# Kernel tuning notes

Measured on AMD Instinct MI355X. Metric: run time of the kernel, lower is better.

Reference implementation:

```python
import jax, jax.numpy as jnp
import numpy as np

NUM_NODES = 6144
INPUT_DIM = 128
OUTPUT_DIM = 128
NUM_HEADS = 4
HEAD_DIM = OUTPUT_DIM // NUM_HEADS
NEG_INF = -9e15  # mask constant used by the original module


def setup_inputs() -> dict:
    key = jax.random.key(0)
    k_x, k_adj, k_W, k_a = jax.random.split(key, 4)
    x = jax.random.normal(k_x, (NUM_NODES, INPUT_DIM), dtype=jnp.float32)
    adj = jax.random.randint(k_adj, (NUM_NODES, NUM_NODES), 0, 2, dtype=jnp.int32)
    # kaiming-uniform-ish init scale
    W = jax.random.uniform(k_W, (NUM_HEADS, INPUT_DIM, HEAD_DIM), dtype=jnp.float32,
                           minval=-1.0, maxval=1.0) * np.sqrt(6.0 / INPUT_DIM)
    a = jax.random.uniform(k_a, (NUM_HEADS, 2 * HEAD_DIM, 1), dtype=jnp.float32,
                           minval=-1.0, maxval=1.0) * np.sqrt(6.0 / (2 * HEAD_DIM))
    return {"x": x, "adj": adj, "W": W, "a": a}


def reference(x, adj, W, a):
    # x: [N, Din], adj: [N, N] int, W: [H, Din, d], a: [H, 2d, 1]
    H, Din, d = W.shape
    N = x.shape[0]
    h = jnp.einsum('ni,hid->hnd', x, W)               # [H, N, d] per-head projections
    a_dst = a[:, :d, 0]                                # applied to h_j (column / source of message)
    a_src = a[:, d:, 0]                                # applied to h_i (row / destination)
    s_dst = jnp.einsum('hnd,hd->hn', h, a_dst)         # [H, N]
    s_src = jnp.einsum('hnd,hd->hn', h, a_src)         # [H, N]
    # energy[h, i, j] = leaky_relu(a1 . h_j + a2 . h_i), same as concat-attention
    energy = jax.nn.leaky_relu(s_src[:, :, None] + s_dst[:, None, :], negative_slope=0.2)
    energy = jnp.where(adj[None] > 0, energy, NEG_INF)  # [H, N, N]
    attention = jax.nn.softmax(energy, axis=-1)
    h_prime = jnp.einsum('hij,hjd->hid', attention, h)  # [H, N, d]
    # faithful to torch h_prime.view(num_nodes, -1) on a contiguous [H,N,d] tensor
    return jnp.reshape(h_prime, (N, H * d))
```

## Files before the change

kernel.cpp:

```cpp
#include <hip/hip_runtime.h>
#include <stdint.h>

#define N_NODES 6144
#define LOG2E 1.44269504088896f

typedef float f32x4 __attribute__((ext_vector_type(4)));
typedef short short8 __attribute__((ext_vector_type(8)));
typedef unsigned int uint32;

extern "C" __device__ float __ocml_native_exp2_f32(float);

__device__ __forceinline__ unsigned int pack2bf(float a, float b) {
  unsigned int ua = __float_as_uint(a) + 0x8000u;
  unsigned int ub = __float_as_uint(b) + 0x8000u;
  return __builtin_amdgcn_perm(ub, ua, 0x07060302u);
}

__global__ __launch_bounds__(256) void k0_pack(const int* __restrict__ adj,
                                               uint32* __restrict__ maskw) {
  unsigned int id = blockIdx.x * 256 + threadIdx.x;
  const int* src = adj + (size_t)id * 32;
  uint32 bits = 0;
  #pragma unroll
  for (int q = 0; q < 8; ++q) {
    int4 v = *(const int4*)(src + q * 4);
    bits |= (v.x != 0 ? 1u : 0u) << (4 * q);
    bits |= (v.y != 0 ? 1u : 0u) << (4 * q + 1);
    bits |= (v.z != 0 ? 1u : 0u) << (4 * q + 2);
    bits |= (v.w != 0 ? 1u : 0u) << (4 * q + 3);
  }
  maskw[id] = bits;
}

__global__ __launch_bounds__(256) void k1_feat(const float* __restrict__ x,
                                               const float* __restrict__ W,
                                               const float* __restrict__ a,
                                               unsigned short* __restrict__ hfT,
                                               float* __restrict__ s_src2,
                                               float* __restrict__ s_dst2) {
  __shared__ float xl[64][132];
  __shared__ float Wl[64][128];
  int t = threadIdx.x;
  int n0 = blockIdx.x * 64;
  for (int u = t; u < 2048; u += 256) {
    int row = u >> 5, c4 = (u & 31) << 2;
    *(float4*)&xl[row][c4] = *(const float4*)(x + (size_t)(n0 + row) * 128 + c4);
  }
  int cg = t & 31, c0 = cg << 2;
  int ng = t >> 5, nb = ng << 3;
  float acc[8][4] = {};
  for (int ic = 0; ic < 2; ++ic) {
    __syncthreads();
    for (int u = t; u < 2048; u += 256) {
      int ii = u >> 5, c4 = (u & 31) << 2;
      int hh = c4 >> 5, d0 = c4 & 31;
      *(float4*)&Wl[ii][c4] = *(const float4*)(W + hh * 4096 + (ic * 64 + ii) * 32 + d0);
    }
    __syncthreads();
    #pragma unroll 4
    for (int ii = 0; ii < 64; ++ii) {
      float4 wv = *(float4*)&Wl[ii][c0];
      int i = ic * 64 + ii;
      #pragma unroll
      for (int r = 0; r < 8; ++r) {
        float xv = xl[nb + r][i];
        acc[r][0] += xv * wv.x; acc[r][1] += xv * wv.y;
        acc[r][2] += xv * wv.z; acc[r][3] += xv * wv.w;
      }
    }
  }
  __syncthreads();
  unsigned short* tb = (unsigned short*)&xl[0][0];
  float* pb = &Wl[0][0];
  int hh = c0 >> 5, d0 = c0 & 31;
  float4 adv = *(const float4*)(a + hh * 64 + d0);
  float4 asv = *(const float4*)(a + hh * 64 + 32 + d0);
  #pragma unroll
  for (int cc = 0; cc < 4; ++cc) {
    unsigned int* dst = (unsigned int*)(tb + (c0 + cc) * 66 + nb);
    #pragma unroll
    for (int p = 0; p < 4; ++p)
      dst[p] = pack2bf(acc[2 * p][cc], acc[2 * p + 1][cc]);
  }
  #pragma unroll
  for (int r = 0; r < 8; ++r) {
    float pd = acc[r][0] * adv.x + acc[r][1] * adv.y + acc[r][2] * adv.z + acc[r][3] * adv.w;
    float ps = acc[r][0] * asv.x + acc[r][1] * asv.y + acc[r][2] * asv.z + acc[r][3] * asv.w;
    pb[(nb + r) * 33 + cg] = pd;
    pb[2112 + (nb + r) * 33 + cg] = ps;
  }
  __syncthreads();
  {
    int row = t >> 1, half = t & 1;
    const unsigned int* s32 = (const unsigned int*)(tb + row * 66 + half * 32);
    unsigned int v[16];
    #pragma unroll
    for (int q = 0; q < 16; ++q) v[q] = s32[q];
    unsigned short* gdst = hfT + (size_t)row * N_NODES + n0 + half * 32;
    #pragma unroll
    for (int q = 0; q < 4; ++q) {
      uint4 w4; w4.x = v[4 * q]; w4.y = v[4 * q + 1]; w4.z = v[4 * q + 2]; w4.w = v[4 * q + 3];
      *(uint4*)(gdst + q * 8) = w4;
    }
  }
  for (int task = t; task < 512; task += 256) {
    int n = task & 63, hz = task >> 6;
    int h = hz & 3, sdx = hz >> 2;
    const float* src = pb + sdx * 2112 + n * 33 + h * 8;
    float s = src[0] + src[1] + src[2] + src[3] + src[4] + src[5] + src[6] + src[7];
    float* out = sdx ? s_src2 : s_dst2;
    out[h * N_NODES + n0 + n] = s * LOG2E;
  }
}

__device__ __forceinline__ void gat_tile(float ss, uint32 bits8,
                                         const float (&dv)[8], short8 b0, short8 b1,
                                         f32x4& a0, f32x4& a1, float& zacc) {
  float w[8];
  #pragma unroll
  for (int j = 0; j < 8; ++j) {
    float e = ss + dv[j];
    float lr = fmaxf(e, 0.2f * e);
    float ex = __ocml_native_exp2_f32(lr);
    w[j] = (bits8 & (1u << j)) ? ex : 0.f;
  }
  zacc += ((w[0] + w[1]) + (w[2] + w[3])) + ((w[4] + w[5]) + (w[6] + w[7]));
  union { uint32 u4[4]; short8 v; } afr;
  #pragma unroll
  for (int j = 0; j < 4; ++j) afr.u4[j] = pack2bf(w[2 * j], w[2 * j + 1]);
  a0 = __builtin_amdgcn_mfma_f32_16x16x32_bf16(afr.v, b0, a0, 0, 0, 0);
  a1 = __builtin_amdgcn_mfma_f32_16x16x32_bf16(afr.v, b1, a1, 0, 0, 0);
}

__device__ __forceinline__ void gat_step4(
    uint32 w0, uint32 w1, uint32 w2, uint32 w3, int sh,
    f32x4 d0, f32x4 d1, int4 B0i, int4 B1i,
    float ss0, float ss1, float ss2, float ss3,
    f32x4& a00, f32x4& a01, f32x4& a10, f32x4& a11,
    f32x4& a20, f32x4& a21, f32x4& a30, f32x4& a31,
    float& z0, float& z1, float& z2, float& z3) {
  float dv[8] = {d0[0], d0[1], d0[2], d0[3], d1[0], d1[1], d1[2], d1[3]};
  union { int4 i; short8 v; } b0u, b1u;
  b0u.i = B0i; b1u.i = B1i;
  gat_tile(ss0, (w0 >> sh) & 0xffu, dv, b0u.v, b1u.v, a00, a01, z0);
  gat_tile(ss1, (w1 >> sh) & 0xffu, dv, b0u.v, b1u.v, a10, a11, z1);
  gat_tile(ss2, (w2 >> sh) & 0xffu, dv, b0u.v, b1u.v, a20, a21, z2);
  gat_tile(ss3, (w3 >> sh) & 0xffu, dv, b0u.v, b1u.v, a30, a31, z3);
}

__global__ __launch_bounds__(256) void k2_attn(const uint32* __restrict__ maskw,
                                               const unsigned short* __restrict__ hfT,
                                               const float* __restrict__ s_src2,
                                               const float* __restrict__ s_dst2,
                                               float* __restrict__ Zpart,
                                               float* __restrict__ part) {
  __shared__ float sd[4][384];
  int t = threadIdx.x;
  int h = t >> 6, lane = t & 63, m = lane & 15, quad = lane >> 4;
  int bx = blockIdx.x;
  int slice = bx & 15, mg = bx >> 4;
  int i0 = mg << 6;
  int kbase = slice * 384;
  {
    const float4* g = (const float4*)s_dst2;
    float4* l = (float4*)sd;
    int kb4 = kbase >> 2;
    for (int u = t; u < 384; u += 256) {
      int hx = u / 96, uu = u - hx * 96;
      l[hx * 96 + uu] = g[hx * 1536 + kb4 + uu];
    }
  }
  float ss0 = s_src2[h * N_NODES + i0 + m];
  float ss1 = s_src2[h * N_NODES + i0 + 16 + m];
  float ss2 = s_src2[h * N_NODES + i0 + 32 + m];
  float ss3 = s_src2[h * N_NODES + i0 + 48 + m];
  __syncthreads();

  int sh = quad << 3;
  const unsigned short* hp0 = hfT + (size_t)(h * 32 + m) * N_NODES + kbase + sh;
  const unsigned short* hp1 = hp0 + (size_t)16 * N_NODES;
  const uint32* mr0 = maskw + (size_t)(i0 + m) * 192 + slice * 12;
  const uint32* mr1 = mr0 + 16 * 192;
  const uint32* mr2 = mr0 + 32 * 192;
  const uint32* mr3 = mr0 + 48 * 192;
  const float* sdh = &sd[h][0];

  f32x4 a00 = {0,0,0,0}, a01 = {0,0,0,0};
  f32x4 a10 = {0,0,0,0}, a11 = {0,0,0,0};
  f32x4 a20 = {0,0,0,0}, a21 = {0,0,0,0};
  f32x4 a30 = {0,0,0,0}, a31 = {0,0,0,0};
  float z0 = 0.f, z1 = 0.f, z2 = 0.f, z3 = 0.f;

  int4 Ba0 = *(const int4*)hp0;
  int4 Ba1 = *(const int4*)hp1;
  uint32 wa0 = mr0[0], wa1 = mr1[0], wa2 = mr2[0], wa3 = mr3[0];
  f32x4 da0 = *(const f32x4*)(sdh + sh);
  f32x4 da1 = *(const f32x4*)(sdh + sh + 4);

  #pragma unroll 1
  for (int it = 0; it < 12; it += 2) {
    int kB = (it + 1) << 5;
    int4 Bb0 = *(const int4*)(hp0 + kB);
    int4 Bb1 = *(const int4*)(hp1 + kB);
    uint32 wb0 = mr0[it + 1], wb1 = mr1[it + 1], wb2 = mr2[it + 1], wb3 = mr3[it + 1];
    f32x4 db0 = *(const f32x4*)(sdh + kB + sh);
    f32x4 db1 = *(const f32x4*)(sdh + kB + sh + 4);
    __builtin_amdgcn_sched_barrier(0);
    gat_step4(wa0, wa1, wa2, wa3, sh, da0, da1, Ba0, Ba1, ss0, ss1, ss2, ss3,
              a00, a01, a10, a11, a20, a21, a30, a31, z0, z1, z2, z3);
    int itn = (it + 2 < 12) ? it + 2 : 0;
    int kA = itn << 5;
    Ba0 = *(const int4*)(hp0 + kA);
    Ba1 = *(const int4*)(hp1 + kA);
    wa0 = mr0[itn]; wa1 = mr1[itn]; wa2 = mr2[itn]; wa3 = mr3[itn];
    da0 = *(const f32x4*)(sdh + kA + sh);
    da1 = *(const f32x4*)(sdh + kA + sh + 4);
    __builtin_amdgcn_sched_barrier(0);
    gat_step4(wb0, wb1, wb2, wb3, sh, db0, db1, Bb0, Bb1, ss0, ss1, ss2, ss3,
              a00, a01, a10, a11, a20, a21, a30, a31, z0, z1, z2, z3);
  }

  z0 += __shfl_xor(z0, 16); z0 += __shfl_xor(z0, 32);
  z1 += __shfl_xor(z1, 16); z1 += __shfl_xor(z1, 32);
  z2 += __shfl_xor(z2, 16); z2 += __shfl_xor(z2, 32);
  z3 += __shfl_xor(z3, 16); z3 += __shfl_xor(z3, 32);
  if (lane < 16) {
    float* zb = Zpart + h * N_NODES + i0 + m;
    atomicAdd(zb, z0);
    atomicAdd(zb + 16, z1);
    atomicAdd(zb + 32, z2);
    atomicAdd(zb + 48, z3);
  }
  float* pb = part + (size_t)h * (N_NODES * 32) + (size_t)i0 * 32;
  #pragma unroll
  for (int r = 0; r < 4; ++r) {
    int row = (quad << 2) + r;
    atomicAdd(&pb[row * 32 + m], a00[r]);
    atomicAdd(&pb[row * 32 + 16 + m], a01[r]);
    atomicAdd(&pb[(16 + row) * 32 + m], a10[r]);
    atomicAdd(&pb[(16 + row) * 32 + 16 + m], a11[r]);
    atomicAdd(&pb[(32 + row) * 32 + m], a20[r]);
    atomicAdd(&pb[(32 + row) * 32 + 16 + m], a21[r]);
    atomicAdd(&pb[(48 + row) * 32 + m], a30[r]);
    atomicAdd(&pb[(48 + row) * 32 + 16 + m], a31[r]);
  }
}

__global__ __launch_bounds__(256) void k3_final(const float* __restrict__ part,
                                                const float* __restrict__ Zpart,
                                                float* __restrict__ out) {
  unsigned int idx4 = blockIdx.x * 256 + threadIdx.x;
  unsigned int h = idx4 / 49152u;
  unsigned int i = (idx4 - h * 49152u) >> 3;
  float rz = 1.0f / Zpart[h * N_NODES + i];
  f32x4 p = ((const f32x4*)part)[idx4];
  ((f32x4*)out)[idx4] = p * rz;
}

extern "C" void kernel_launch(void* const* d_in, const int* in_sizes, int n_in,
                              void* d_out, int out_size, void* d_ws, size_t ws_size,
                              hipStream_t stream) {
  const float* x = (const float*)d_in[0];
  const int* adj = (const int*)d_in[1];
  const float* W = (const float*)d_in[2];
  const float* a = (const float*)d_in[3];
  float* out = (float*)d_out;

  float* wsf = (float*)d_ws;
  unsigned short* hfT = (unsigned short*)wsf;
  float* s_src2 = wsf + 393216;
  float* s_dst2 = s_src2 + 24576;
  float* part   = s_dst2 + 24576;
  float* Zpart  = part + 786432;
  uint32* maskw = (uint32*)(Zpart + 24576);

  (void)hipMemsetAsync(part, 0, (786432 + 24576) * sizeof(float), stream);
  hipLaunchKernelGGL(k0_pack, dim3(4608), dim3(256), 0, stream, adj, maskw);
  hipLaunchKernelGGL(k1_feat, dim3(96), dim3(256), 0, stream, x, W, a, hfT, s_src2, s_dst2);
  hipLaunchKernelGGL(k2_attn, dim3(1536), dim3(256), 0, stream,
                     maskw, hfT, s_src2, s_dst2, Zpart, part);
  hipLaunchKernelGGL(k3_final, dim3(768), dim3(256), 0, stream, part, Zpart, out);
}
```

Baseline: 309.0 us.

## Fuse adjacency bitmask packing into attention kernel with LDS-staged tiles

Removes the separate adjacency-packing kernel and packs the int32 adjacency rows into bitmasks inside the attention kernel, so the packed mask is never written to or re-read from global memory. The attention kernel now stages the bf16 feature tile, the mask words and the destination scores in shared memory in chunks of 256 columns, and covers twice as many columns per block with half as many blocks. This saves one launch and the mask round-trip through global memory. In exchange it adds syncthreads per chunk, drops the explicit register double-buffered prefetch, and uses roughly 70KB of LDS per block, which can lower occupancy. The adjacency read (about 150MB) still dominates the runtime.

Result: no change. 311.5 us (+0.8%).

```diff
diff --git a/kernel.cpp b/kernel.cpp
--- a/kernel.cpp
+++ b/kernel.cpp
@@ -14,22 +14,6 @@
   unsigned int ua = __float_as_uint(a) + 0x8000u;
   unsigned int ub = __float_as_uint(b) + 0x8000u;
   return __builtin_amdgcn_perm(ub, ua, 0x07060302u);
-}
-
-__global__ __launch_bounds__(256) void k0_pack(const int* __restrict__ adj,
-                                               uint32* __restrict__ maskw) {
-  unsigned int id = blockIdx.x * 256 + threadIdx.x;
-  const int* src = adj + (size_t)id * 32;
-  uint32 bits = 0;
-  #pragma unroll
-  for (int q = 0; q < 8; ++q) {
-    int4 v = *(const int4*)(src + q * 4);
-    bits |= (v.x != 0 ? 1u : 0u) << (4 * q);
-    bits |= (v.y != 0 ? 1u : 0u) << (4 * q + 1);
-    bits |= (v.z != 0 ? 1u : 0u) << (4 * q + 2);
-    bits |= (v.w != 0 ? 1u : 0u) << (4 * q + 3);
-  }
-  maskw[id] = bits;
 }
 
 __global__ __launch_bounds__(256) void k1_feat(const float* __restrict__ x,
@@ -132,58 +116,27 @@
   a1 = __builtin_amdgcn_mfma_f32_16x16x32_bf16(afr.v, b1, a1, 0, 0, 0);
 }
 
-__device__ __forceinline__ void gat_step4(
-    uint32 w0, uint32 w1, uint32 w2, uint32 w3, int sh,
-    f32x4 d0, f32x4 d1, int4 B0i, int4 B1i,
-    float ss0, float ss1, float ss2, float ss3,
-    f32x4& a00, f32x4& a01, f32x4& a10, f32x4& a11,
-    f32x4& a20, f32x4& a21, f32x4& a30, f32x4& a31,
-    float& z0, float& z1, float& z2, float& z3) {
-  float dv[8] = {d0[0], d0[1], d0[2], d0[3], d1[0], d1[1], d1[2], d1[3]};
-  union { int4 i; short8 v; } b0u, b1u;
-  b0u.i = B0i; b1u.i = B1i;
-  gat_tile(ss0, (w0 >> sh) & 0xffu, dv, b0u.v, b1u.v, a00, a01, z0);
-  gat_tile(ss1, (w1 >> sh) & 0xffu, dv, b0u.v, b1u.v, a10, a11, z1);
-  gat_tile(ss2, (w2 >> sh) & 0xffu, dv, b0u.v, b1u.v, a20, a21, z2);
-  gat_tile(ss3, (w3 >> sh) & 0xffu, dv, b0u.v, b1u.v, a30, a31, z3);
-}
-
-__global__ __launch_bounds__(256) void k2_attn(const uint32* __restrict__ maskw,
+__global__ __launch_bounds__(256) void k2_attn(const int* __restrict__ adj,
                                                const unsigned short* __restrict__ hfT,
                                                const float* __restrict__ s_src2,
                                                const float* __restrict__ s_dst2,
                                                float* __restrict__ Zpart,
                                                float* __restrict__ part) {
-  __shared__ float sd[4][384];
+  __shared__ unsigned short hfl[128 * 264];
+  __shared__ uint32 ml[64 * 9];
+  __shared__ float sdl[4 * 256];
   int t = threadIdx.x;
   int h = t >> 6, lane = t & 63, m = lane & 15, quad = lane >> 4;
+  int sh = quad << 3;
   int bx = blockIdx.x;
-  int slice = bx & 15, mg = bx >> 4;
+  int slice = bx & 7, mg = bx >> 3;
   int i0 = mg << 6;
-  int kbase = slice * 384;
-  {
-    const float4* g = (const float4*)s_dst2;
-    float4* l = (float4*)sd;
-    int kb4 = kbase >> 2;
-    for (int u = t; u < 384; u += 256) {
-      int hx = u / 96, uu = u - hx * 96;
-      l[hx * 96 + uu] = g[hx * 1536 + kb4 + uu];
-    }
-  }
+  int kb0 = slice * 768;
+
   float ss0 = s_src2[h * N_NODES + i0 + m];
   float ss1 = s_src2[h * N_NODES + i0 + 16 + m];
   float ss2 = s_src2[h * N_NODES + i0 + 32 + m];
   float ss3 = s_src2[h * N_NODES + i0 + 48 + m];
-  __syncthreads();
-
-  int sh = quad << 3;
-  const unsigned short* hp0 = hfT + (size_t)(h * 32 + m) * N_NODES + kbase + sh;
-  const unsigned short* hp1 = hp0 + (size_t)16 * N_NODES;
-  const uint32* mr0 = maskw + (size_t)(i0 + m) * 192 + slice * 12;
-  const uint32* mr1 = mr0 + 16 * 192;
-  const uint32* mr2 = mr0 + 32 * 192;
-  const uint32* mr3 = mr0 + 48 * 192;
-  const float* sdh = &sd[h][0];
 
   f32x4 a00 = {0,0,0,0}, a01 = {0,0,0,0};
   f32x4 a10 = {0,0,0,0}, a11 = {0,0,0,0};
@@ -191,33 +144,72 @@
   f32x4 a30 = {0,0,0,0}, a31 = {0,0,0,0};
   float z0 = 0.f, z1 = 0.f, z2 = 0.f, z3 = 0.f;
 
-  int4 Ba0 = *(const int4*)hp0;
-  int4 Ba1 = *(const int4*)hp1;
-  uint32 wa0 = mr0[0], wa1 = mr1[0], wa2 = mr2[0], wa3 = mr3[0];
-  f32x4 da0 = *(const f32x4*)(sdh + sh);
-  f32x4 da1 = *(const f32x4*)(sdh + sh + 4);
-
-  #pragma unroll 1
-  for (int it = 0; it < 12; it += 2) {
-    int kB = (it + 1) << 5;
-    int4 Bb0 = *(const int4*)(hp0 + kB);
-    int4 Bb1 = *(const int4*)(hp1 + kB);
-    uint32 wb0 = mr0[it + 1], wb1 = mr1[it + 1], wb2 = mr2[it + 1], wb3 = mr3[it + 1];
-    f32x4 db0 = *(const f32x4*)(sdh + kB + sh);
-    f32x4 db1 = *(const f32x4*)(sdh + kB + sh + 4);
-    __builtin_amdgcn_sched_barrier(0);
-    gat_step4(wa0, wa1, wa2, wa3, sh, da0, da1, Ba0, Ba1, ss0, ss1, ss2, ss3,
-              a00, a01, a10, a11, a20, a21, a30, a31, z0, z1, z2, z3);
-    int itn = (it + 2 < 12) ? it + 2 : 0;
-    int kA = itn << 5;
-    Ba0 = *(const int4*)(hp0 + kA);
-    Ba1 = *(const int4*)(hp1 + kA);
-    wa0 = mr0[itn]; wa1 = mr1[itn]; wa2 = mr2[itn]; wa3 = mr3[itn];
-    da0 = *(const f32x4*)(sdh + kA + sh);
-    da1 = *(const f32x4*)(sdh + kA + sh + 4);
-    __builtin_amdgcn_sched_barrier(0);
-    gat_step4(wb0, wb1, wb2, wb3, sh, db0, db1, Bb0, Bb1, ss0, ss1, ss2, ss3,
-              a00, a01, a10, a11, a20, a21, a30, a31, z0, z1, z2, z3);
+  int s_row = t >> 1, s_half = t & 1;
+  int a_row = t >> 2, a_wq = t & 3;
+  int d_h = t >> 6, d_k = (t & 63) << 2;
+
+  for (int c = 0; c < 3; ++c) {
+    int kb = kb0 + (c << 8);
+    if (c) __syncthreads();
+    {
+      const unsigned short* g = hfT + (size_t)s_row * N_NODES + kb + (s_half << 7);
+      unsigned short* l = hfl + s_row * 264 + (s_half << 7);
+      #pragma unroll
+      for (int i = 0; i < 16; ++i)
+        *(int4*)(l + (i << 3)) = *(const int4*)(g + (i << 3));
+    }
+    {
+      const int* g = adj + (size_t)(i0 + a_row) * N_NODES + kb + (a_wq << 6);
+      uint32 w0 = 0, w1 = 0;
+      #pragma unroll
+      for (int i = 0; i < 8; ++i) {
+        int4 v = *(const int4*)(g + (i << 2));
+        int bb = i << 2;
+        w0 |= (v.x != 0 ? 1u : 0u) << bb;
+        w0 |= (v.y != 0 ? 1u : 0u) << (bb + 1);
+        w0 |= (v.z != 0 ? 1u : 0u) << (bb + 2);
+        w0 |= (v.w != 0 ? 1u : 0u) << (bb + 3);
+      }
+      #pragma unroll
+      for (int i = 8; i < 16; ++i) {
+        int4 v = *(const int4*)(g + (i << 2));
+        int bb = (i - 8) << 2;
+        w1 |= (v.x != 0 ? 1u : 0u) << bb;
+        w1 |= (v.y != 0 ? 1u : 0u) << (bb + 1);
+        w1 |= (v.z != 0 ? 1u : 0u) << (bb + 2);
+        w1 |= (v.w != 0 ? 1u : 0u) << (bb + 3);
+      }
+      ml[a_row * 9 + (a_wq << 1)] = w0;
+      ml[a_row * 9 + (a_wq << 1) + 1] = w1;
+    }
+    *(float4*)&sdl[d_h * 256 + d_k] =
+        *(const float4*)(s_dst2 + d_h * N_NODES + kb + d_k);
+    __syncthreads();
+
+    const unsigned short* hb0 = hfl + (h * 32 + m) * 264 + sh;
+    const unsigned short* hb1 = hb0 + 16 * 264;
+    const float* sdp = sdl + h * 256 + sh;
+    const uint32* m0p = ml + (0 * 16 + m) * 9;
+    const uint32* m1p = ml + (1 * 16 + m) * 9;
+    const uint32* m2p = ml + (2 * 16 + m) * 9;
+    const uint32* m3p = ml + (3 * 16 + m) * 9;
+    #pragma unroll
+    for (int kt = 0; kt < 8; ++kt) {
+      union { int4 i; short8 v; } b0u, b1u;
+      b0u.i = *(const int4*)(hb0 + (kt << 5));
+      b1u.i = *(const int4*)(hb1 + (kt << 5));
+      f32x4 dd0 = *(const f32x4*)(sdp + (kt << 5));
+      f32x4 dd1 = *(const f32x4*)(sdp + (kt << 5) + 4);
+      float dv[8] = {dd0[0], dd0[1], dd0[2], dd0[3], dd1[0], dd1[1], dd1[2], dd1[3]};
+      uint32 w0 = (m0p[kt] >> sh) & 0xffu;
+      uint32 w1 = (m1p[kt] >> sh) & 0xffu;
+      uint32 w2 = (m2p[kt] >> sh) & 0xffu;
+      uint32 w3 = (m3p[kt] >> sh) & 0xffu;
+      gat_tile(ss0, w0, dv, b0u.v, b1u.v, a00, a01, z0);
+      gat_tile(ss1, w1, dv, b0u.v, b1u.v, a10, a11, z1);
+      gat_tile(ss2, w2, dv, b0u.v, b1u.v, a20, a21, z2);
+      gat_tile(ss3, w3, dv, b0u.v, b1u.v, a30, a31, z3);
+    }
   }
 
   z0 += __shfl_xor(z0, 16); z0 += __shfl_xor(z0, 32);
@@ -272,12 +264,10 @@
   float* s_dst2 = s_src2 + 24576;
   float* part   = s_dst2 + 24576;
   float* Zpart  = part + 786432;
-  uint32* maskw = (uint32*)(Zpart + 24576);
 
   (void)hipMemsetAsync(part, 0, (786432 + 24576) * sizeof(float), stream);
-  hipLaunchKernelGGL(k0_pack, dim3(4608), dim3(256), 0, stream, adj, maskw);
   hipLaunchKernelGGL(k1_feat, dim3(96), dim3(256), 0, stream, x, W, a, hfT, s_src2, s_dst2);
-  hipLaunchKernelGGL(k2_attn, dim3(1536), dim3(256), 0, stream,
-                     maskw, hfT, s_src2, s_dst2, Zpart, part);
+  hipLaunchKernelGGL(k2_attn, dim3(768), dim3(256), 0, stream,
+                     adj, hfT, s_src2, s_dst2, Zpart, part);
   hipLaunchKernelGGL(k3_final, dim3(768), dim3(256), 0, stream, part, Zpart, out);
 }
```

## Pack mask via wave ballot, compute row sums with MFMA, widen attention k-slices

Applied to the files above, without the earlier changes.

The mask packing now uses a wavefront ballot. Each wave reads one adjacency row with coalesced per-lane loads and emits 64-bit words. The bit order changes accordingly, and the attention kernel reinterprets it as 32-bit words. The attention kernel takes k-slices twice as wide (768 columns), with half as many blocks and half the partial-sum atomics. Loads are batched four steps at a time with vectorized mask reads. The softmax denominator is now computed by an extra MFMA against a ones vector instead of scalar adds plus shuffles. This trades more MFMA work and register pressure (launch bounds 3) for fewer VALU ops and atomics.

Result: slower. 317.7 us (+2.8%).

```diff
diff --git a/kernel.cpp b/kernel.cpp
--- a/kernel.cpp
+++ b/kernel.cpp
@@ -7,6 +7,7 @@
 typedef float f32x4 __attribute__((ext_vector_type(4)));
 typedef short short8 __attribute__((ext_vector_type(8)));
 typedef unsigned int uint32;
+typedef unsigned long long uint64;
 
 extern "C" __device__ float __ocml_native_exp2_f32(float);
 
@@ -17,19 +18,18 @@
 }
 
 __global__ __launch_bounds__(256) void k0_pack(const int* __restrict__ adj,
-                                               uint32* __restrict__ maskw) {
-  unsigned int id = blockIdx.x * 256 + threadIdx.x;
-  const int* src = adj + (size_t)id * 32;
-  uint32 bits = 0;
-  #pragma unroll
-  for (int q = 0; q < 8; ++q) {
-    int4 v = *(const int4*)(src + q * 4);
-    bits |= (v.x != 0 ? 1u : 0u) << (4 * q);
-    bits |= (v.y != 0 ? 1u : 0u) << (4 * q + 1);
-    bits |= (v.z != 0 ? 1u : 0u) << (4 * q + 2);
-    bits |= (v.w != 0 ? 1u : 0u) << (4 * q + 3);
-  }
-  maskw[id] = bits;
+                                               uint64* __restrict__ mask64) {
+  int t = threadIdx.x;
+  int wid = t >> 6, lane = t & 63;
+  int row = blockIdx.x * 4 + wid;
+  const int* ar = adj + (size_t)row * N_NODES + lane;
+  uint64* mr = mask64 + (size_t)row * 96;
+  #pragma unroll 8
+  for (int c = 0; c < 96; ++c) {
+    int v = ar[c << 6];
+    uint64 b = __ballot(v != 0);
+    if (lane == (c & 63)) mr[c] = b;
+  }
 }
 
 __global__ __launch_bounds__(256) void k1_feat(const float* __restrict__ x,
@@ -115,7 +115,7 @@
 
 __device__ __forceinline__ void gat_tile(float ss, uint32 bits8,
                                          const float (&dv)[8], short8 b0, short8 b1,
-                                         f32x4& a0, f32x4& a1, float& zacc) {
+                                         short8 ones, f32x4& a0, f32x4& a1, f32x4& az) {
   float w[8];
   #pragma unroll
   for (int j = 0; j < 8; ++j) {
@@ -124,50 +124,54 @@
     float ex = __ocml_native_exp2_f32(lr);
     w[j] = (bits8 & (1u << j)) ? ex : 0.f;
   }
-  zacc += ((w[0] + w[1]) + (w[2] + w[3])) + ((w[4] + w[5]) + (w[6] + w[7]));
   union { uint32 u4[4]; short8 v; } afr;
   #pragma unroll
   for (int j = 0; j < 4; ++j) afr.u4[j] = pack2bf(w[2 * j], w[2 * j + 1]);
   a0 = __builtin_amdgcn_mfma_f32_16x16x32_bf16(afr.v, b0, a0, 0, 0, 0);
   a1 = __builtin_amdgcn_mfma_f32_16x16x32_bf16(afr.v, b1, a1, 0, 0, 0);
-}
-
-__device__ __forceinline__ void gat_step4(
-    uint32 w0, uint32 w1, uint32 w2, uint32 w3, int sh,
-    f32x4 d0, f32x4 d1, int4 B0i, int4 B1i,
-    float ss0, float ss1, float ss2, float ss3,
-    f32x4& a00, f32x4& a01, f32x4& a10, f32x4& a11,
-    f32x4& a20, f32x4& a21, f32x4& a30, f32x4& a31,
-    float& z0, float& z1, float& z2, float& z3) {
+  az = __builtin_amdgcn_mfma_f32_16x16x32_bf16(afr.v, ones, az, 0, 0, 0);
+}
+
+__device__ __forceinline__ void step4(uint32 w0, uint32 w1, uint32 w2, uint32 w3,
+                                      int sh, const float* sdp, int koff,
+                                      int4 B0i, int4 B1i, short8 ones,
+                                      float ss0, float ss1, float ss2, float ss3,
+                                      f32x4& a00, f32x4& a01, f32x4& a10, f32x4& a11,
+                                      f32x4& a20, f32x4& a21, f32x4& a30, f32x4& a31,
+                                      f32x4& az0, f32x4& az1, f32x4& az2, f32x4& az3) {
+  f32x4 d0 = *(const f32x4*)(sdp + koff);
+  f32x4 d1 = *(const f32x4*)(sdp + koff + 4);
   float dv[8] = {d0[0], d0[1], d0[2], d0[3], d1[0], d1[1], d1[2], d1[3]};
   union { int4 i; short8 v; } b0u, b1u;
   b0u.i = B0i; b1u.i = B1i;
-  gat_tile(ss0, (w0 >> sh) & 0xffu, dv, b0u.v, b1u.v, a00, a01, z0);
-  gat_tile(ss1, (w1 >> sh) & 0xffu, dv, b0u.v, b1u.v, a10, a11, z1);
-  gat_tile(ss2, (w2 >> sh) & 0xffu, dv, b0u.v, b1u.v, a20, a21, z2);
-  gat_tile(ss3, (w3 >> sh) & 0xffu, dv, b0u.v, b1u.v, a30, a31, z3);
-}
-
-__global__ __launch_bounds__(256) void k2_attn(const uint32* __restrict__ maskw,
-                                               const unsigned short* __restrict__ hfT,
-                                               const float* __restrict__ s_src2,
-                                               const float* __restrict__ s_dst2,
-                                               float* __restrict__ Zpart,
-                                               float* __restrict__ part) {
-  __shared__ float sd[4][384];
+  gat_tile(ss0, (w0 >> sh) & 0xffu, dv, b0u.v, b1u.v, ones, a00, a01, az0);
+  gat_tile(ss1, (w1 >> sh) & 0xffu, dv, b0u.v, b1u.v, ones, a10, a11, az1);
+  gat_tile(ss2, (w2 >> sh) & 0xffu, dv, b0u.v, b1u.v, ones, a20, a21, az2);
+  gat_tile(ss3, (w3 >> sh) & 0xffu, dv, b0u.v, b1u.v, ones, a30, a31, az3);
+}
+
+__global__ __launch_bounds__(256, 3) void k2_attn(const uint32* __restrict__ maskw,
+                                                  const unsigned short* __restrict__ hfT,
+                                                  const float* __restrict__ s_src2,
+                                                  const float* __restrict__ s_dst2,
+                                                  float* __restrict__ Zpart,
+                                                  float* __restrict__ part) {
+  __shared__ float sd[4][768];
   int t = threadIdx.x;
   int h = t >> 6, lane = t & 63, m = lane & 15, quad = lane >> 4;
+  int sh = quad << 3;
   int bx = blockIdx.x;
-  int slice = bx & 15, mg = bx >> 4;
-  int i0 = mg << 6;
-  int kbase = slice * 384;
+  int slice = bx & 7, mg = bx >> 3;
+  int i0 = mg << 6, kbase = slice * 768;
   {
     const float4* g = (const float4*)s_dst2;
     float4* l = (float4*)sd;
     int kb4 = kbase >> 2;
-    for (int u = t; u < 384; u += 256) {
-      int hx = u / 96, uu = u - hx * 96;
-      l[hx * 96 + uu] = g[hx * 1536 + kb4 + uu];
+    #pragma unroll
+    for (int r = 0; r < 3; ++r) {
+      int u = t + (r << 8);
+      int hx = u / 192, uu = u - hx * 192;
+      l[hx * 192 + uu] = g[hx * 1536 + kb4 + uu];
     }
   }
   float ss0 = s_src2[h * N_NODES + i0 + m];
@@ -176,60 +180,59 @@
   float ss3 = s_src2[h * N_NODES + i0 + 48 + m];
   __syncthreads();
 
-  int sh = quad << 3;
   const unsigned short* hp0 = hfT + (size_t)(h * 32 + m) * N_NODES + kbase + sh;
   const unsigned short* hp1 = hp0 + (size_t)16 * N_NODES;
-  const uint32* mr0 = maskw + (size_t)(i0 + m) * 192 + slice * 12;
+  const uint32* mr0 = maskw + (size_t)(i0 + m) * 192 + slice * 24;
   const uint32* mr1 = mr0 + 16 * 192;
   const uint32* mr2 = mr0 + 32 * 192;
   const uint32* mr3 = mr0 + 48 * 192;
-  const float* sdh = &sd[h][0];
+  const float* sdp = &sd[h][0] + sh;
 
   f32x4 a00 = {0,0,0,0}, a01 = {0,0,0,0};
   f32x4 a10 = {0,0,0,0}, a11 = {0,0,0,0};
   f32x4 a20 = {0,0,0,0}, a21 = {0,0,0,0};
   f32x4 a30 = {0,0,0,0}, a31 = {0,0,0,0};
-  float z0 = 0.f, z1 = 0.f, z2 = 0.f, z3 = 0.f;
-
-  int4 Ba0 = *(const int4*)hp0;
-  int4 Ba1 = *(const int4*)hp1;
-  uint32 wa0 = mr0[0], wa1 = mr1[0], wa2 = mr2[0], wa3 = mr3[0];
-  f32x4 da0 = *(const f32x4*)(sdh + sh);
-  f32x4 da1 = *(const f32x4*)(sdh + sh + 4);
+  f32x4 az0 = {0,0,0,0}, az1 = {0,0,0,0};
+  f32x4 az2 = {0,0,0,0}, az3 = {0,0,0,0};
+  union { uint32 u[4]; short8 v; } ones;
+  #pragma unroll
+  for (int q = 0; q < 4; ++q) ones.u[q] = 0x3F803F80u;
 
   #pragma unroll 1
-  for (int it = 0; it < 12; it += 2) {
-    int kB = (it + 1) << 5;
-    int4 Bb0 = *(const int4*)(hp0 + kB);
-    int4 Bb1 = *(const int4*)(hp1 + kB);
-    uint32 wb0 = mr0[it + 1], wb1 = mr1[it + 1], wb2 = mr2[it + 1], wb3 = mr3[it + 1];
-    f32x4 db0 = *(const f32x4*)(sdh + kB + sh);
-    f32x4 db1 = *(const f32x4*)(sdh + kB + sh + 4);
+  for (int o = 0; o < 6; ++o) {
+    int ko = o << 7;
+    uint4 M0 = *(const uint4*)(mr0 + (o << 2));
+    uint4 M1 = *(const uint4*)(mr1 + (o << 2));
+    uint4 M2 = *(const uint4*)(mr2 + (o << 2));
+    uint4 M3 = *(const uint4*)(mr3 + (o << 2));
+    int4 B00 = *(const int4*)(hp0 + ko),      B01 = *(const int4*)(hp1 + ko);
+    int4 B10 = *(const int4*)(hp0 + ko + 32), B11 = *(const int4*)(hp1 + ko + 32);
+    int4 B20 = *(const int4*)(hp0 + ko + 64), B21 = *(const int4*)(hp1 + ko + 64);
+    int4 B30 = *(const int4*)(hp0 + ko + 96), B31 = *(const int4*)(hp1 + ko + 96);
     __builtin_amdgcn_sched_barrier(0);
-    gat_step4(wa0, wa1, wa2, wa3, sh, da0, da1, Ba0, Ba1, ss0, ss1, ss2, ss3,
-              a00, a01, a10, a11, a20, a21, a30, a31, z0, z1, z2, z3);
-    int itn = (it + 2 < 12) ? it + 2 : 0;
-    int kA = itn << 5;
-    Ba0 = *(const int4*)(hp0 + kA);
-    Ba1 = *(const int4*)(hp1 + kA);
-    wa0 = mr0[itn]; wa1 = mr1[itn]; wa2 = mr2[itn]; wa3 = mr3[itn];
-    da0 = *(const f32x4*)(sdh + kA + sh);
-    da1 = *(const f32x4*)(sdh + kA + sh + 4);
-    __builtin_amdgcn_sched_barrier(0);
-    gat_step4(wb0, wb1, wb2, wb3, sh, db0, db1, Bb0, Bb1, ss0, ss1, ss2, ss3,
-              a00, a01, a10, a11, a20, a21, a30, a31, z0, z1, z2, z3);
-  }
-
-  z0 += __shfl_xor(z0, 16); z0 += __shfl_xor(z0, 32);
-  z1 += __shfl_xor(z1, 16); z1 += __shfl_xor(z1, 32);
-  z2 += __shfl_xor(z2, 16); z2 += __shfl_xor(z2, 32);
-  z3 += __shfl_xor(z3, 16); z3 += __shfl_xor(z3, 32);
-  if (lane < 16) {
-    float* zb = Zpart + h * N_NODES + i0 + m;
-    atomicAdd(zb, z0);
-    atomicAdd(zb + 16, z1);
-    atomicAdd(zb + 32, z2);
-    atomicAdd(zb + 48, z3);
+    step4(M0.x, M1.x, M2.x, M3.x, sh, sdp, ko,      B00, B01, ones.v,
+          ss0, ss1, ss2, ss3, a00, a01, a10, a11, a20, a21, a30, a31,
+          az0, az1, az2, az3);
+    step4(M0.y, M1.y, M2.y, M3.y, sh, sdp, ko + 32, B10, B11, ones.v,
+          ss0, ss1, ss2, ss3, a00, a01, a10, a11, a20, a21, a30, a31,
+          az0, az1, az2, az3);
+    step4(M0.z, M1.z, M2.z, M3.z, sh, sdp, ko + 64, B20, B21, ones.v,
+          ss0, ss1, ss2, ss3, a00, a01, a10, a11, a20, a21, a30, a31,
+          az0, az1, az2, az3);
+    step4(M0.w, M1.w, M2.w, M3.w, sh, sdp, ko + 96, B30, B31, ones.v,
+          ss0, ss1, ss2, ss3, a00, a01, a10, a11, a20, a21, a30, a31,
+          az0, az1, az2, az3);
+  }
+
+  if (m == 0) {
+    float* zb = Zpart + h * N_NODES + i0 + (quad << 2);
+    #pragma unroll
+    for (int r = 0; r < 4; ++r) {
+      atomicAdd(zb + r, az0[r]);
+      atomicAdd(zb + 16 + r, az1[r]);
+      atomicAdd(zb + 32 + r, az2[r]);
+      atomicAdd(zb + 48 + r, az3[r]);
+    }
   }
   float* pb = part + (size_t)h * (N_NODES * 32) + (size_t)i0 * 32;
   #pragma unroll
@@ -272,12 +275,12 @@
   float* s_dst2 = s_src2 + 24576;
   float* part   = s_dst2 + 24576;
   float* Zpart  = part + 786432;
-  uint32* maskw = (uint32*)(Zpart + 24576);
+  uint64* mask64 = (uint64*)(Zpart + 24576);
 
   (void)hipMemsetAsync(part, 0, (786432 + 24576) * sizeof(float), stream);
-  hipLaunchKernelGGL(k0_pack, dim3(4608), dim3(256), 0, stream, adj, maskw);
+  hipLaunchKernelGGL(k0_pack, dim3(1536), dim3(256), 0, stream, adj, mask64);
   hipLaunchKernelGGL(k1_feat, dim3(96), dim3(256), 0, stream, x, W, a, hfT, s_src2, s_dst2);
-  hipLaunchKernelGGL(k2_attn, dim3(1536), dim3(256), 0, stream,
-                     maskw, hfT, s_src2, s_dst2, Zpart, part);
+  hipLaunchKernelGGL(k2_attn, dim3(768), dim3(256), 0, stream,
+                     (const uint32*)mask64, hfT, s_src2, s_dst2, Zpart, part);
   hipLaunchKernelGGL(k3_final, dim3(768), dim3(256), 0, stream, part, Zpart, out);
 }
```
